# Optimization experiments

Measured on AMD Instinct MI355X. Metric: run time of the kernel, lower is better.

The kernel has to match this reference:

```python
import jax, jax.numpy as jnp
import numpy as np

K = 20  # number of unrolled recurrent steps


def setup_inputs() -> dict:
    key = jax.random.key(0)
    k_w, k_b, k0, k1, kv = jax.random.split(key, 5)
    B, d, h = 4096, 128, 256
    w = jax.random.normal(k_w, (B, d, d), dtype=jnp.float32) * 0.05
    b = jax.random.normal(k_b, (B, d), dtype=jnp.float32)
    W0 = jax.random.normal(k0, (h, 2 * d), dtype=jnp.float32) * 0.05
    W1 = jax.random.normal(k1, (h, h), dtype=jnp.float32) * 0.05
    V = jax.random.normal(kv, (d, h), dtype=jnp.float32) * 0.05
    return {"w": w, "b": b, "W0": W0, "W1": W1, "V": V}


def _cell(x, w, b, W0, W1, V):
    # gradient = w @ x - b  -> [B, d]
    grad = jnp.einsum('bij,bj->bi', w, x) - b
    h = jnp.concatenate([-grad, x], axis=-1)      # [B, 2d]
    h = jax.nn.relu(h @ W0.T)                     # [B, h0]
    h = jax.nn.relu(h @ W1.T)                     # [B, h1]
    return h @ V.T                                # [B, d]


def reference(w, b, W0, W1, V):
    x0 = jnp.zeros_like(b)

    def step(x, _):
        return _cell(x, w, b, W0, W1, V), None

    x, _ = jax.lax.scan(step, x0, None, length=K)
    return x
```

## Files before the change

### kernel.cpp

```cpp
#include <hip/hip_runtime.h>
#include <stdint.h>

#define KSTEPS 20
#define EPB 4
#define NBLOCKS 1024
#define NTHREADS 512

#define WQ_OFF     0
#define HB_OFF     131072
#define H0B_OFF    133248
#define H1B_OFF    135424
#define SMEM_BYTES 137600

#define ACT_STRIDE 544

typedef short bf16x8 __attribute__((ext_vector_type(8)));
typedef float f32x4  __attribute__((ext_vector_type(4)));

static __device__ __forceinline__ uint32_t f2bf(float x) {
    union { float f; uint32_t u; } v; v.f = x;
    return (v.u + 0x7fffu + ((v.u >> 16) & 1u)) >> 16;
}
static __device__ __forceinline__ uint32_t packbf2(float a, float b) {
    return f2bf(a) | (f2bf(b) << 16);
}

__global__ void prep_kernel(const float* __restrict__ W0, const float* __restrict__ W1,
                            const float* __restrict__ V, uint16_t* __restrict__ out)
{
    int i = blockIdx.x * 256 + threadIdx.x;
    float v;
    if (i < 65536) {
        int c = i >> 11, rest = i & 2047, r = rest >> 3, m = rest & 7;
        v = W0[r * 256 + c * 8 + m];
    } else if (i < 131072) {
        int j = i - 65536;
        int c = j >> 11, rest = j & 2047, r = rest >> 3, m = rest & 7;
        v = W1[r * 256 + c * 8 + m];
    } else {
        int j = i - 131072;
        int c = j >> 10, rest = j & 1023, r = rest >> 3, m = rest & 7;
        v = V[r * 256 + c * 8 + m];
    }
    out[i] = (uint16_t)f2bf(v);
}

__global__
__attribute__((amdgpu_flat_work_group_size(512, 512), amdgpu_waves_per_eu(2, 2)))
void mlprnn_main(
    const float* __restrict__ w, const float* __restrict__ b,
    const uint16_t* __restrict__ wp, float* __restrict__ out)
{
    extern __shared__ char smem[];

    const int t  = threadIdx.x;
    const int e0 = blockIdx.x * EPB;

    const int l = t & 63, wv = t >> 6;
    const int row15 = l & 15;
    const int kg    = l >> 4;
    const int cm    = l & 3;
    const bool cok  = row15 < 4;
    const int mt0 = 2 * wv, mt1 = 2 * wv + 1;

    const int e_g  = wv >> 1;
    const int mh   = wv & 1;

    const bf16x8* w0v = (const bf16x8*)wp;
    const bf16x8* w1v = w0v + 32 * 256;
    const bf16x8* vv  = w1v + 32 * 256;

    bf16x8 a0w[8], a1w[8], b0w[8], b1w[8], vw[8];
    #pragma unroll
    for (int kk = 0; kk < 8; ++kk) {
        a0w[kk] = w0v[(kk * 4 + kg) * 256 + mt0 * 16 + row15];
        a1w[kk] = w0v[(kk * 4 + kg) * 256 + mt1 * 16 + row15];
        b0w[kk] = w1v[(kk * 4 + kg) * 256 + mt0 * 16 + row15];
        b1w[kk] = w1v[(kk * 4 + kg) * 256 + mt1 * 16 + row15];
        vw[kk]  = vv[(kk * 4 + kg) * 128 + wv * 16 + row15];
    }
    f32x4 bseed[4];
    #pragma unroll
    for (int mt = 0; mt < 4; ++mt)
        bseed[mt] = *(const f32x4*)(b + (size_t)(e0 + e_g) * 128 + mh * 64 + mt * 16 + kg * 4);

    {
        const float4* wg = (const float4*)w;
        for (int it = 0; it < 32; ++it) {
            int g  = it * NTHREADS + t;
            int e  = g >> 12;
            int gg = g & 4095;
            int r  = gg >> 5, q = gg & 31;
            float4 f = wg[(size_t)(e0 + e) * 4096 + gg];
            uint2 pk = { packbf2(-f.x, -f.y), packbf2(-f.z, -f.w) };
            int byte = e * 32768 + r * 256 + q * 8;
            byte ^= (r & 7) << 4;
            *(uint2*)(smem + WQ_OFF + byte) = pk;
        }
    }
    {
        int bi = t >> 7, r = t & 127;
        *(uint16_t*)(smem + HB_OFF + bi * ACT_STRIDE + 256 + 2 * r) = 0;
    }
    __syncthreads();

    const char* wqA = smem + WQ_OFF + e_g * 32768 + (mh * 64 + row15) * 256;
    const int   wqx = (row15 & 7) << 4;
    const char* xB  = smem + HB_OFF + e_g * ACT_STRIDE + 256 + kg * 16;

    const char* hbB = smem + HB_OFF  + cm * ACT_STRIDE + kg * 16;
    const char* h0B = smem + H0B_OFF + cm * ACT_STRIDE + kg * 16;
    const char* h1B = smem + H1B_OFF + cm * ACT_STRIDE + kg * 16;

    for (int k = 0; k < KSTEPS; ++k) {
        {
            bf16x8 bx[4];
            #pragma unroll
            for (int kt = 0; kt < 4; ++kt)
                bx[kt] = *(const bf16x8*)(xB + kt * 64);

            f32x4 ag0 = bseed[0], ag1 = bseed[1], ag2 = bseed[2], ag3 = bseed[3];
            #pragma unroll
            for (int kt = 0; kt < 4; ++kt) {
                bf16x8 a0 = *(const bf16x8*)(wqA + ((0 * 16) * 256 + kt * 64 + kg * 16 ^ wqx));
                bf16x8 a1 = *(const bf16x8*)(wqA + ((1 * 16) * 256 + kt * 64 + kg * 16 ^ wqx));
                bf16x8 a2 = *(const bf16x8*)(wqA + ((2 * 16) * 256 + kt * 64 + kg * 16 ^ wqx));
                bf16x8 a3 = *(const bf16x8*)(wqA + ((3 * 16) * 256 + kt * 64 + kg * 16 ^ wqx));
                ag0 = __builtin_amdgcn_mfma_f32_16x16x32_bf16(a0, bx[kt], ag0, 0, 0, 0);
                ag1 = __builtin_amdgcn_mfma_f32_16x16x32_bf16(a1, bx[kt], ag1, 0, 0, 0);
                ag2 = __builtin_amdgcn_mfma_f32_16x16x32_bf16(a2, bx[kt], ag2, 0, 0, 0);
                ag3 = __builtin_amdgcn_mfma_f32_16x16x32_bf16(a3, bx[kt], ag3, 0, 0, 0);
            }
            char* gw = smem + HB_OFF + e_g * ACT_STRIDE;
            if (row15 == 0) *(uint2*)(gw + (mh * 64 + 0 * 16 + kg * 4) * 2)
                = (uint2){ packbf2(ag0[0], ag0[1]), packbf2(ag0[2], ag0[3]) };
            if (row15 == 1) *(uint2*)(gw + (mh * 64 + 1 * 16 + kg * 4) * 2)
                = (uint2){ packbf2(ag1[0], ag1[1]), packbf2(ag1[2], ag1[3]) };
            if (row15 == 2) *(uint2*)(gw + (mh * 64 + 2 * 16 + kg * 4) * 2)
                = (uint2){ packbf2(ag2[0], ag2[1]), packbf2(ag2[2], ag2[3]) };
            if (row15 == 3) *(uint2*)(gw + (mh * 64 + 3 * 16 + kg * 4) * 2)
                = (uint2){ packbf2(ag3[0], ag3[1]), packbf2(ag3[2], ag3[3]) };
        }
        __syncthreads();

        {
            f32x4 acc0 = {0.f, 0.f, 0.f, 0.f};
            f32x4 acc1 = {0.f, 0.f, 0.f, 0.f};
            #pragma unroll
            for (int kk = 0; kk < 8; ++kk) {
                bf16x8 bf = *(const bf16x8*)(hbB + kk * 64);
                acc0 = __builtin_amdgcn_mfma_f32_16x16x32_bf16(a0w[kk], bf, acc0, 0, 0, 0);
                acc1 = __builtin_amdgcn_mfma_f32_16x16x32_bf16(a1w[kk], bf, acc1, 0, 0, 0);
            }
            if (cok) {
                uint2 q0 = { packbf2(fmaxf(acc0[0], 0.f), fmaxf(acc0[1], 0.f)),
                             packbf2(fmaxf(acc0[2], 0.f), fmaxf(acc0[3], 0.f)) };
                uint2 q1 = { packbf2(fmaxf(acc1[0], 0.f), fmaxf(acc1[1], 0.f)),
                             packbf2(fmaxf(acc1[2], 0.f), fmaxf(acc1[3], 0.f)) };
                *(uint2*)(smem + H0B_OFF + row15 * ACT_STRIDE + (mt0 * 16 + kg * 4) * 2) = q0;
                *(uint2*)(smem + H0B_OFF + row15 * ACT_STRIDE + (mt1 * 16 + kg * 4) * 2) = q1;
            }
            __syncthreads();
        }

        {
            f32x4 acc0 = {0.f, 0.f, 0.f, 0.f};
            f32x4 acc1 = {0.f, 0.f, 0.f, 0.f};
            #pragma unroll
            for (int kk = 0; kk < 8; ++kk) {
                bf16x8 bf = *(const bf16x8*)(h0B + kk * 64);
                acc0 = __builtin_amdgcn_mfma_f32_16x16x32_bf16(b0w[kk], bf, acc0, 0, 0, 0);
                acc1 = __builtin_amdgcn_mfma_f32_16x16x32_bf16(b1w[kk], bf, acc1, 0, 0, 0);
            }
            if (cok) {
                uint2 q0 = { packbf2(fmaxf(acc0[0], 0.f), fmaxf(acc0[1], 0.f)),
                             packbf2(fmaxf(acc0[2], 0.f), fmaxf(acc0[3], 0.f)) };
                uint2 q1 = { packbf2(fmaxf(acc1[0], 0.f), fmaxf(acc1[1], 0.f)),
                             packbf2(fmaxf(acc1[2], 0.f), fmaxf(acc1[3], 0.f)) };
                *(uint2*)(smem + H1B_OFF + row15 * ACT_STRIDE + (mt0 * 16 + kg * 4) * 2) = q0;
                *(uint2*)(smem + H1B_OFF + row15 * ACT_STRIDE + (mt1 * 16 + kg * 4) * 2) = q1;
            }
            __syncthreads();
        }

        {
            f32x4 acc = {0.f, 0.f, 0.f, 0.f};
            #pragma unroll
            for (int kk = 0; kk < 8; ++kk) {
                bf16x8 bf = *(const bf16x8*)(h1B + kk * 64);
                acc = __builtin_amdgcn_mfma_f32_16x16x32_bf16(vw[kk], bf, acc, 0, 0, 0);
            }
            if (cok) {
                const int r = wv * 16 + kg * 4;
                uint2 q = { packbf2(acc[0], acc[1]), packbf2(acc[2], acc[3]) };
                *(uint2*)(smem + HB_OFF + row15 * ACT_STRIDE + 256 + r * 2) = q;
                if (k == KSTEPS - 1) {
                    *(f32x4*)(&out[(size_t)(e0 + row15) * 128 + r]) = acc;
                }
            }
            __syncthreads();
        }
    }
}

extern "C" void kernel_launch(void* const* d_in, const int* in_sizes, int n_in,
                              void* d_out, int out_size, void* d_ws, size_t ws_size,
                              hipStream_t stream)
{
    const float* w  = (const float*)d_in[0];
    const float* b  = (const float*)d_in[1];
    const float* W0 = (const float*)d_in[2];
    const float* W1 = (const float*)d_in[3];
    const float* V  = (const float*)d_in[4];
    float* out = (float*)d_out;
    uint16_t* wp = (uint16_t*)d_ws;

    prep_kernel<<<640, 256, 0, stream>>>(W0, W1, V, wp);

    hipFuncSetAttribute((const void*)mlprnn_main,
                        hipFuncAttributeMaxDynamicSharedMemorySize, SMEM_BYTES);
    mlprnn_main<<<NBLOCKS, NTHREADS, SMEM_BYTES, stream>>>(w, b, wp, out);
}
```

Measured before the change: 218.3 us.

## Peel first step using known grad and overlap w staging with MLP phases

Measured after the change: 202.7 us. -7.1%, faster.

```diff
diff --git a/kernel.cpp b/kernel.cpp
--- a/kernel.cpp
+++ b/kernel.cpp
@@ -6,11 +6,13 @@
 #define NBLOCKS 1024
 #define NTHREADS 512
 
-#define WQ_OFF     0
-#define HB_OFF     131072
-#define H0B_OFF    133248
-#define H1B_OFF    135424
-#define SMEM_BYTES 137600
+#define WQ_E_STRIDE 33792
+#define FB_STRIDE   1056
+#define WQ_OFF      0
+#define HB_OFF      135168
+#define H0B_OFF     137344
+#define H1B_OFF     139520
+#define SMEM_BYTES  141696
 
 #define ACT_STRIDE 544
 
@@ -85,121 +87,116 @@
         bseed[mt] = *(const f32x4*)(b + (size_t)(e0 + e_g) * 128 + mh * 64 + mt * 16 + kg * 4);
 
     {
-        const float4* wg = (const float4*)w;
-        for (int it = 0; it < 32; ++it) {
-            int g  = it * NTHREADS + t;
-            int e  = g >> 12;
-            int gg = g & 4095;
-            int r  = gg >> 5, q = gg & 31;
-            float4 f = wg[(size_t)(e0 + e) * 4096 + gg];
-            uint2 pk = { packbf2(-f.x, -f.y), packbf2(-f.z, -f.w) };
-            int byte = e * 32768 + r * 256 + q * 8;
-            byte ^= (r & 7) << 4;
-            *(uint2*)(smem + WQ_OFF + byte) = pk;
-        }
-    }
-    {
-        int bi = t >> 7, r = t & 127;
-        *(uint16_t*)(smem + HB_OFF + bi * ACT_STRIDE + 256 + 2 * r) = 0;
+        int e = t >> 7, feat = t & 127;
+        float bv = b[(size_t)(e0 + e) * 128 + feat];
+        *(uint16_t*)(smem + HB_OFF + e * ACT_STRIDE + feat * 2) = (uint16_t)f2bf(bv);
+        *(uint16_t*)(smem + HB_OFF + e * ACT_STRIDE + 256 + feat * 2) = 0;
     }
     __syncthreads();
 
-    const char* wqA = smem + WQ_OFF + e_g * 32768 + (mh * 64 + row15) * 256;
-    const int   wqx = (row15 & 7) << 4;
+    #define STAGE_CHUNK(C) do {                                                   \
+        const float4* wg_ = (const float4*)w;                                     \
+        _Pragma("unroll")                                                         \
+        for (int it = (C) * 8; it < (C) * 8 + 8; ++it) {                          \
+            int g  = it * NTHREADS + t;                                           \
+            int e  = g >> 12;                                                     \
+            int gg = g & 4095;                                                    \
+            int r  = gg >> 5, q = gg & 31;                                        \
+            float4 f = wg_[(size_t)(e0 + e) * 4096 + gg];                         \
+            uint2 pk = { packbf2(-f.x, -f.y), packbf2(-f.z, -f.w) };              \
+            int kt_s = q >> 3, kg_s = (q >> 1) & 3, h = q & 1;                    \
+            int fb   = (r >> 4) * 4 + kt_s;                                       \
+            int byte = e * WQ_E_STRIDE + fb * FB_STRIDE                           \
+                     + (kg_s * 16 + (r & 15)) * 16 + h * 8;                       \
+            *(uint2*)(smem + WQ_OFF + byte) = pk;                                 \
+        }                                                                         \
+    } while (0)
+
+    const char* wqA = smem + WQ_OFF + e_g * WQ_E_STRIDE + l * 16;
     const char* xB  = smem + HB_OFF + e_g * ACT_STRIDE + 256 + kg * 16;
 
     const char* hbB = smem + HB_OFF  + cm * ACT_STRIDE + kg * 16;
     const char* h0B = smem + H0B_OFF + cm * ACT_STRIDE + kg * 16;
     const char* h1B = smem + H1B_OFF + cm * ACT_STRIDE + kg * 16;
 
-    for (int k = 0; k < KSTEPS; ++k) {
-        {
-            bf16x8 bx[4];
-            #pragma unroll
-            for (int kt = 0; kt < 4; ++kt)
-                bx[kt] = *(const bf16x8*)(xB + kt * 64);
-
-            f32x4 ag0 = bseed[0], ag1 = bseed[1], ag2 = bseed[2], ag3 = bseed[3];
-            #pragma unroll
-            for (int kt = 0; kt < 4; ++kt) {
-                bf16x8 a0 = *(const bf16x8*)(wqA + ((0 * 16) * 256 + kt * 64 + kg * 16 ^ wqx));
-                bf16x8 a1 = *(const bf16x8*)(wqA + ((1 * 16) * 256 + kt * 64 + kg * 16 ^ wqx));
-                bf16x8 a2 = *(const bf16x8*)(wqA + ((2 * 16) * 256 + kt * 64 + kg * 16 ^ wqx));
-                bf16x8 a3 = *(const bf16x8*)(wqA + ((3 * 16) * 256 + kt * 64 + kg * 16 ^ wqx));
-                ag0 = __builtin_amdgcn_mfma_f32_16x16x32_bf16(a0, bx[kt], ag0, 0, 0, 0);
-                ag1 = __builtin_amdgcn_mfma_f32_16x16x32_bf16(a1, bx[kt], ag1, 0, 0, 0);
-                ag2 = __builtin_amdgcn_mfma_f32_16x16x32_bf16(a2, bx[kt], ag2, 0, 0, 0);
-                ag3 = __builtin_amdgcn_mfma_f32_16x16x32_bf16(a3, bx[kt], ag3, 0, 0, 0);
-            }
-            char* gw = smem + HB_OFF + e_g * ACT_STRIDE;
-            if (row15 == 0) *(uint2*)(gw + (mh * 64 + 0 * 16 + kg * 4) * 2)
-                = (uint2){ packbf2(ag0[0], ag0[1]), packbf2(ag0[2], ag0[3]) };
-            if (row15 == 1) *(uint2*)(gw + (mh * 64 + 1 * 16 + kg * 4) * 2)
-                = (uint2){ packbf2(ag1[0], ag1[1]), packbf2(ag1[2], ag1[3]) };
-            if (row15 == 2) *(uint2*)(gw + (mh * 64 + 2 * 16 + kg * 4) * 2)
-                = (uint2){ packbf2(ag2[0], ag2[1]), packbf2(ag2[2], ag2[3]) };
-            if (row15 == 3) *(uint2*)(gw + (mh * 64 + 3 * 16 + kg * 4) * 2)
-                = (uint2){ packbf2(ag3[0], ag3[1]), packbf2(ag3[2], ag3[3]) };
-        }
-        __syncthreads();
-
-        {
-            f32x4 acc0 = {0.f, 0.f, 0.f, 0.f};
-            f32x4 acc1 = {0.f, 0.f, 0.f, 0.f};
-            #pragma unroll
-            for (int kk = 0; kk < 8; ++kk) {
-                bf16x8 bf = *(const bf16x8*)(hbB + kk * 64);
-                acc0 = __builtin_amdgcn_mfma_f32_16x16x32_bf16(a0w[kk], bf, acc0, 0, 0, 0);
-                acc1 = __builtin_amdgcn_mfma_f32_16x16x32_bf16(a1w[kk], bf, acc1, 0, 0, 0);
-            }
-            if (cok) {
-                uint2 q0 = { packbf2(fmaxf(acc0[0], 0.f), fmaxf(acc0[1], 0.f)),
-                             packbf2(fmaxf(acc0[2], 0.f), fmaxf(acc0[3], 0.f)) };
-                uint2 q1 = { packbf2(fmaxf(acc1[0], 0.f), fmaxf(acc1[1], 0.f)),
-                             packbf2(fmaxf(acc1[2], 0.f), fmaxf(acc1[3], 0.f)) };
-                *(uint2*)(smem + H0B_OFF + row15 * ACT_STRIDE + (mt0 * 16 + kg * 4) * 2) = q0;
-                *(uint2*)(smem + H0B_OFF + row15 * ACT_STRIDE + (mt1 * 16 + kg * 4) * 2) = q1;
-            }
-            __syncthreads();
-        }
-
-        {
-            f32x4 acc0 = {0.f, 0.f, 0.f, 0.f};
-            f32x4 acc1 = {0.f, 0.f, 0.f, 0.f};
-            #pragma unroll
-            for (int kk = 0; kk < 8; ++kk) {
-                bf16x8 bf = *(const bf16x8*)(h0B + kk * 64);
-                acc0 = __builtin_amdgcn_mfma_f32_16x16x32_bf16(b0w[kk], bf, acc0, 0, 0, 0);
-                acc1 = __builtin_amdgcn_mfma_f32_16x16x32_bf16(b1w[kk], bf, acc1, 0, 0, 0);
-            }
-            if (cok) {
-                uint2 q0 = { packbf2(fmaxf(acc0[0], 0.f), fmaxf(acc0[1], 0.f)),
-                             packbf2(fmaxf(acc0[2], 0.f), fmaxf(acc0[3], 0.f)) };
-                uint2 q1 = { packbf2(fmaxf(acc1[0], 0.f), fmaxf(acc1[1], 0.f)),
-                             packbf2(fmaxf(acc1[2], 0.f), fmaxf(acc1[3], 0.f)) };
-                *(uint2*)(smem + H1B_OFF + row15 * ACT_STRIDE + (mt0 * 16 + kg * 4) * 2) = q0;
-                *(uint2*)(smem + H1B_OFF + row15 * ACT_STRIDE + (mt1 * 16 + kg * 4) * 2) = q1;
-            }
-            __syncthreads();
-        }
-
-        {
-            f32x4 acc = {0.f, 0.f, 0.f, 0.f};
-            #pragma unroll
-            for (int kk = 0; kk < 8; ++kk) {
-                bf16x8 bf = *(const bf16x8*)(h1B + kk * 64);
-                acc = __builtin_amdgcn_mfma_f32_16x16x32_bf16(vw[kk], bf, acc, 0, 0, 0);
-            }
-            if (cok) {
-                const int r = wv * 16 + kg * 4;
-                uint2 q = { packbf2(acc[0], acc[1]), packbf2(acc[2], acc[3]) };
-                *(uint2*)(smem + HB_OFF + row15 * ACT_STRIDE + 256 + r * 2) = q;
-                if (k == KSTEPS - 1) {
-                    *(f32x4*)(&out[(size_t)(e0 + row15) * 128 + r]) = acc;
-                }
-            }
-            __syncthreads();
-        }
+    #define PHASE_GRAD() do {                                                     \
+        bf16x8 bx[4];                                                             \
+        _Pragma("unroll")                                                         \
+        for (int kt = 0; kt < 4; ++kt) bx[kt] = *(const bf16x8*)(xB + kt * 64);   \
+        f32x4 ag0 = bseed[0], ag1 = bseed[1], ag2 = bseed[2], ag3 = bseed[3];     \
+        _Pragma("unroll")                                                         \
+        for (int kt = 0; kt < 4; ++kt) {                                          \
+            bf16x8 a0 = *(const bf16x8*)(wqA + (((mh * 4 + 0) * 4 + kt) * FB_STRIDE)); \
+            bf16x8 a1 = *(const bf16x8*)(wqA + (((mh * 4 + 1) * 4 + kt) * FB_STRIDE)); \
+            bf16x8 a2 = *(const bf16x8*)(wqA + (((mh * 4 + 2) * 4 + kt) * FB_STRIDE)); \
+            bf16x8 a3 = *(const bf16x8*)(wqA + (((mh * 4 + 3) * 4 + kt) * FB_STRIDE)); \
+            ag0 = __builtin_amdgcn_mfma_f32_16x16x32_bf16(a0, bx[kt], ag0, 0, 0, 0); \
+            ag1 = __builtin_amdgcn_mfma_f32_16x16x32_bf16(a1, bx[kt], ag1, 0, 0, 0); \
+            ag2 = __builtin_amdgcn_mfma_f32_16x16x32_bf16(a2, bx[kt], ag2, 0, 0, 0); \
+            ag3 = __builtin_amdgcn_mfma_f32_16x16x32_bf16(a3, bx[kt], ag3, 0, 0, 0); \
+        }                                                                         \
+        char* gw = smem + HB_OFF + e_g * ACT_STRIDE;                              \
+        if (row15 == 0) *(uint2*)(gw + (mh * 64 + 0 * 16 + kg * 4) * 2)           \
+            = (uint2){ packbf2(ag0[0], ag0[1]), packbf2(ag0[2], ag0[3]) };        \
+        if (row15 == 1) *(uint2*)(gw + (mh * 64 + 1 * 16 + kg * 4) * 2)           \
+            = (uint2){ packbf2(ag1[0], ag1[1]), packbf2(ag1[2], ag1[3]) };        \
+        if (row15 == 2) *(uint2*)(gw + (mh * 64 + 2 * 16 + kg * 4) * 2)           \
+            = (uint2){ packbf2(ag2[0], ag2[1]), packbf2(ag2[2], ag2[3]) };        \
+        if (row15 == 3) *(uint2*)(gw + (mh * 64 + 3 * 16 + kg * 4) * 2)           \
+            = (uint2){ packbf2(ag3[0], ag3[1]), packbf2(ag3[2], ag3[3]) };        \
+    } while (0)
+
+    #define PHASE_MLP(SRC, AW0, AW1, DST, RELU) do {                              \
+        f32x4 acc0 = {0.f, 0.f, 0.f, 0.f};                                        \
+        f32x4 acc1 = {0.f, 0.f, 0.f, 0.f};                                        \
+        _Pragma("unroll")                                                         \
+        for (int kk = 0; kk < 8; ++kk) {                                          \
+            bf16x8 bf = *(const bf16x8*)((SRC) + kk * 64);                        \
+            acc0 = __builtin_amdgcn_mfma_f32_16x16x32_bf16(AW0[kk], bf, acc0, 0, 0, 0); \
+            acc1 = __builtin_amdgcn_mfma_f32_16x16x32_bf16(AW1[kk], bf, acc1, 0, 0, 0); \
+        }                                                                         \
+        if (cok) {                                                                \
+            uint2 q0 = { packbf2(fmaxf(acc0[0], 0.f), fmaxf(acc0[1], 0.f)),       \
+                         packbf2(fmaxf(acc0[2], 0.f), fmaxf(acc0[3], 0.f)) };     \
+            uint2 q1 = { packbf2(fmaxf(acc1[0], 0.f), fmaxf(acc1[1], 0.f)),       \
+                         packbf2(fmaxf(acc1[2], 0.f), fmaxf(acc1[3], 0.f)) };     \
+            *(uint2*)(smem + (DST) + row15 * ACT_STRIDE + (mt0 * 16 + kg * 4) * 2) = q0; \
+            *(uint2*)(smem + (DST) + row15 * ACT_STRIDE + (mt1 * 16 + kg * 4) * 2) = q1; \
+        }                                                                         \
+    } while (0)
+
+    #define PHASE_V(K) do {                                                       \
+        f32x4 acc = {0.f, 0.f, 0.f, 0.f};                                         \
+        _Pragma("unroll")                                                         \
+        for (int kk = 0; kk < 8; ++kk) {                                          \
+            bf16x8 bf = *(const bf16x8*)(h1B + kk * 64);                          \
+            acc = __builtin_amdgcn_mfma_f32_16x16x32_bf16(vw[kk], bf, acc, 0, 0, 0); \
+        }                                                                         \
+        if (cok) {                                                                \
+            const int r = wv * 16 + kg * 4;                                       \
+            uint2 q = { packbf2(acc[0], acc[1]), packbf2(acc[2], acc[3]) };       \
+            *(uint2*)(smem + HB_OFF + row15 * ACT_STRIDE + 256 + r * 2) = q;      \
+            if ((K) == KSTEPS - 1) {                                              \
+                *(f32x4*)(&out[(size_t)(e0 + row15) * 128 + r]) = acc;            \
+            }                                                                     \
+        }                                                                         \
+    } while (0)
+
+    STAGE_CHUNK(0);
+    PHASE_MLP(hbB, a0w, a1w, H0B_OFF, 1); __syncthreads();
+    STAGE_CHUNK(1);
+    PHASE_MLP(h0B, b0w, b1w, H1B_OFF, 1); __syncthreads();
+    STAGE_CHUNK(2);
+    PHASE_V(0); __syncthreads();
+    STAGE_CHUNK(3);
+    __syncthreads();
+
+    #pragma unroll 1
+    for (int k = 1; k < KSTEPS; ++k) {
+        PHASE_GRAD(); __syncthreads();
+        PHASE_MLP(hbB, a0w, a1w, H0B_OFF, 1); __syncthreads();
+        PHASE_MLP(h0B, b0w, b1w, H1B_OFF, 1); __syncthreads();
+        PHASE_V(k); __syncthreads();
     }
 }
 
```
